# Kernel optimization log

Hardware: AMD Instinct MI355X
Metric: run time of the kernel (lower is better)

The kernel has to match this reference:

```python
import jax, jax.numpy as jnp
import numpy as np
from jax import lax

B, C_IN = 8192, 1

def _conv(x, w, b):
    # x: [N,C,H,W], w: [O,I,kh,kw] valid conv, stride 1
    y = lax.conv_general_dilated(x, w, window_strides=(1, 1), padding='VALID',
                                 dimension_numbers=('NCHW', 'OIHW', 'NCHW'))
    return y + b[None, :, None, None]

def _maxpool2(x):
    return lax.reduce_window(x, -jnp.inf, lax.max, (1, 1, 2, 2), (1, 1, 2, 2), 'VALID')

def setup_inputs() -> dict:
    key = jax.random.key(0)
    ks = jax.random.split(key, 9)
    def kaiming(k, shape, fan_in):
        return jax.random.normal(k, shape, jnp.float32) * np.float32(1.0 / np.sqrt(fan_in))
    x = jax.random.normal(ks[0], (B, C_IN, 28, 28), jnp.float32)
    w1 = kaiming(ks[1], (10, C_IN, 5, 5), C_IN * 25)
    b1 = kaiming(ks[2], (10,), C_IN * 25)
    w2 = kaiming(ks[3], (20, 10, 5, 5), 10 * 25)
    b2 = kaiming(ks[4], (20,), 10 * 25)
    wl1 = kaiming(ks[5], (50, 320), 320)
    bl1 = kaiming(ks[6], (50,), 320)
    wl2 = kaiming(ks[7], (10, 50), 50)
    bl2 = kaiming(ks[8], (10,), 50)
    return {"x": x, "w1": w1, "b1": b1, "w2": w2, "b2": b2,
            "wl1": wl1, "bl1": bl1, "wl2": wl2, "bl2": bl2}

def reference(x, w1, b1, w2, b2, wl1, bl1, wl2, bl2):
    h = jax.nn.relu(_conv(x, w1, b1))       # [B,10,24,24]
    h = _maxpool2(h)                         # [B,10,12,12]
    h = jax.nn.relu(_conv(h, w2, b2))        # [B,20,8,8]
    h = _maxpool2(h)                         # [B,20,4,4]
    h = h.reshape(h.shape[0], -1)            # [B,320]
    h = jax.nn.relu(h @ wl1.T + bl1)         # [B,50]
    return h @ wl2.T + bl2                   # [B,10]
```

## Files before the change

### kernel.cpp

```cpp
#include <hip/hip_runtime.h>

#define THREADS 256
#define IPB 4

typedef _Float16 f16;
typedef _Float16 f16x2 __attribute__((ext_vector_type(2)));
typedef _Float16 f16x8 __attribute__((ext_vector_type(8)));
typedef float f32x2 __attribute__((ext_vector_type(2)));
typedef float f32x4 __attribute__((ext_vector_type(4)));
typedef float f32x16 __attribute__((ext_vector_type(16)));
typedef unsigned int uint;

__device__ __forceinline__ f16x2 pkrtz(float a, float b) {
    return __builtin_bit_cast(f16x2, __builtin_amdgcn_cvt_pkrtz(a, b));
}
template<int CTRL>
__device__ __forceinline__ float dppmax(float v) {
    const int i = __builtin_bit_cast(int, v);
    const int s = __builtin_amdgcn_update_dpp(i, i, CTRL, 0xF, 0xF, true);
    return fmaxf(v, __builtin_bit_cast(float, s));
}

#define P1_ROW 400
#define P1_IMG 4784
#define SMEM_BYTES 19136

__global__ void pack_weights(const float* __restrict__ w1,
                             const float* __restrict__ w2,
                             const float* __restrict__ wl1,
                             unsigned char* __restrict__ ws) {
    uint* w1pk  = (uint*)ws;
    f16x8* w2af = (f16x8*)(ws + 1024);
    f16x8* wl1pk = (f16x8*)(ws + 17408);
    const int gid = blockIdx.x * blockDim.x + threadIdx.x;
    const int gsz = gridDim.x * blockDim.x;
    for (int i = gid; i < 250; i += gsz) {
        const unsigned short u =
            __builtin_bit_cast(unsigned short, (f16)w1[i]);
        w1pk[i] = (uint)u | ((uint)u << 16);
    }
    for (int e = gid; e < 1000; e += gsz) {
        const int s = e / 40, r = e - s * 40;
        const int oc = r >> 1, h = r & 1;
        f16x8 a;
        #pragma unroll
        for (int j = 0; j < 8; ++j) {
            const int ic = h * 8 + j;
            a[j] = (f16)(ic < 10 ? w2[(oc * 10 + ic) * 25 + s] : 0.f);
        }
        w2af[e] = a;
    }
    for (int e = gid; e < 2560; e += gsz) {
        const int tile = e / 640, rem = e % 640;
        const int s = rem / 64, lane = rem % 64;
        const int m = lane & 15, quad = lane >> 4;
        const int hh = tile * 16 + m;
        f16x8 a;
        #pragma unroll
        for (int j = 0; j < 8; ++j)
            a[j] = (f16)(hh < 50 ? wl1[hh * 320 + s * 32 + quad * 8 + j] : 0.f);
        wl1pk[e] = a;
    }
}

__global__ __launch_bounds__(THREADS, 8)
void lenet_one(const float* __restrict__ x,
               const unsigned char* __restrict__ ws, const float* __restrict__ b1,
               const float* __restrict__ b2,
               const float* __restrict__ bl1,
               const float* __restrict__ wl2, const float* __restrict__ bl2,
               float* __restrict__ out, int batch)
{
    __shared__ __align__(16) unsigned char p1c[SMEM_BYTES];
    f16*   p2h = (f16*)p1c;
    float* h1  = (float*)(p1c + 2624);

    const uint*  w1pk  = (const uint*)ws;
    const f16x8* w2af  = (const f16x8*)(ws + 1024);
    const f16x8* wl1pk = (const f16x8*)(ws + 17408);

    const int tid = threadIdx.x;
    const int lane = tid & 63;
    const int wv_ = tid >> 6;
    const int cM = lane & 31, hK = lane >> 5;
    const int img = tid & 3;
    const int imgg = min(blockIdx.x * IPB + img, batch - 1);

    {
        const int grp = tid >> 2;
        const float* xim = x + (size_t)imgg * 784;
        for (int pq = grp; pq < 144; pq += 64) {
            const int py = pq / 12, px = pq % 12;
            const float* xb = xim + (2 * py) * 28 + 2 * px;
            f16x2 accT[10], accB[10];
            #pragma unroll
            for (int c = 0; c < 10; ++c) {
                accT[c] = {(f16)0.f, (f16)0.f};
                accB[c] = {(f16)0.f, (f16)0.f};
            }
            #pragma unroll
            for (int r = 0; r < 6; ++r) {
                const f32x2 a01 = *(const f32x2*)(xb + r * 28);
                const f32x2 a23 = *(const f32x2*)(xb + r * 28 + 2);
                const f32x2 a45 = *(const f32x2*)(xb + r * 28 + 4);
                f16x2 p[5];
                p[0] = pkrtz(a01[0], a01[1]);
                p[1] = pkrtz(a01[1], a23[0]);
                p[2] = pkrtz(a23[0], a23[1]);
                p[3] = pkrtz(a23[1], a45[0]);
                p[4] = pkrtz(a45[0], a45[1]);
                #pragma unroll
                for (int c = 0; c < 10; ++c) {
                    #pragma unroll
                    for (int kx = 0; kx < 5; ++kx) {
                        if (r < 5) {
                            const f16x2 wv = __builtin_bit_cast(
                                f16x2, w1pk[c * 25 + r * 5 + kx]);
                            accT[c] += p[kx] * wv;
                        }
                        if (r >= 1) {
                            const f16x2 wv = __builtin_bit_cast(
                                f16x2, w1pk[c * 25 + (r - 1) * 5 + kx]);
                            accB[c] += p[kx] * wv;
                        }
                    }
                }
            }
            f16 ch[10];
            #pragma unroll
            for (int c = 0; c < 10; ++c) {
                const float q0 = fmaxf((float)accT[c][0], (float)accB[c][0]);
                const float q1 = fmaxf((float)accT[c][1], (float)accB[c][1]);
                ch[c] = (f16)fmaxf(fmaxf(q0, q1) + b1[c], 0.f);
            }
            f16x8 v0, v1;
            #pragma unroll
            for (int j = 0; j < 8; ++j) v0[j] = ch[j];
            v1[0] = ch[8]; v1[1] = ch[9];
            #pragma unroll
            for (int j = 2; j < 8; ++j) v1[j] = (f16)0.f;
            unsigned char* dst = p1c + img * P1_IMG + py * P1_ROW + px * 32;
            *(f16x8*)(dst)      = v0;
            *(f16x8*)(dst + 16) = v1;
        }
    }
    __syncthreads();

    {
        const int cy = cM >> 3, cx = cM & 7;
        const int afoff = (cM < 20 ? cM : 19) * 2 + hK;
        int bb[2];
        #pragma unroll
        for (int q = 0; q < 2; ++q) {
            const int t = wv_ * 2 + q, im = t >> 1, h2 = t & 1;
            bb[q] = im * P1_IMG + (4 * h2 + cy) * P1_ROW + cx * 32 + hK * 16;
        }
        f32x16 acc[2];
        #pragma unroll
        for (int q = 0; q < 2; ++q)
            #pragma unroll
            for (int r = 0; r < 16; ++r) acc[q][r] = 0.f;
        #pragma unroll 1
        for (int ky = 0; ky < 5; ++ky) {
            #pragma unroll
            for (int kx = 0; kx < 5; ++kx) {
                const f16x8 a = w2af[(ky * 5 + kx) * 40 + afoff];
                #pragma unroll
                for (int q = 0; q < 2; ++q) {
                    const f16x8 b =
                        *(const f16x8*)(p1c + bb[q] + ky * P1_ROW + kx * 32);
                    acc[q] = __builtin_amdgcn_mfma_f32_32x32x16_f16(a, b, acc[q],
                                                                    0, 0, 0);
                }
            }
        }
        __syncthreads();
        #pragma unroll
        for (int q = 0; q < 2; ++q) {
            const int t = wv_ * 2 + q, im = t >> 1, h2 = t & 1;
            #pragma unroll
            for (int r = 0; r < 16; ++r) {
                const int m = (r & 3) + 8 * (r >> 2) + 4 * hK;
                float v = acc[q][r];
                v = dppmax<0xB1>(v);
                v = dppmax<0x128>(v);
                if (m < 20 && (lane & 9) == 0) {
                    const int py = 2 * h2 + (cM >> 4), px = cx >> 1;
                    p2h[im * 328 + m * 16 + py * 4 + px] =
                        (f16)fmaxf(v + b2[m], 0.f);
                }
            }
        }
    }
    __syncthreads();

    {
        const int n = lane & 15, quad = lane >> 4;
        f32x4 facc = {0.f, 0.f, 0.f, 0.f};
        #pragma unroll 1
        for (int s = 0; s < 10; ++s) {
            const f16x8 a = wl1pk[(wv_ * 10 + s) * 64 + lane];
            f16x8 b = {};
            if (n < IPB)
                b = *(const f16x8*)(p2h + n * 328 + s * 32 + quad * 8);
            facc = __builtin_amdgcn_mfma_f32_16x16x32_f16(a, b, facc, 0, 0, 0);
        }
        if (n < IPB) {
            #pragma unroll
            for (int r = 0; r < 4; ++r) {
                const int h = wv_ * 16 + quad * 4 + r;
                if (h < 50)
                    h1[n * 52 + h] = fmaxf(facc[r] + bl1[h], 0.f);
            }
        }
    }
    __syncthreads();

    if (tid < IPB * 10) {
        const int im = tid / 10, o = tid % 10;
        const int imgo = min(blockIdx.x * IPB + im, batch - 1);
        float a = bl2[o];
        #pragma unroll
        for (int h = 0; h < 50; ++h)
            a += h1[im * 52 + h] * wl2[o * 50 + h];
        out[(size_t)imgo * 10 + o] = a;
    }
}

extern "C" void kernel_launch(void* const* d_in, const int* in_sizes, int n_in,
                              void* d_out, int out_size, void* d_ws, size_t ws_size,
                              hipStream_t stream) {
    const float* x   = (const float*)d_in[0];
    const float* w1  = (const float*)d_in[1];
    const float* b1  = (const float*)d_in[2];
    const float* w2  = (const float*)d_in[3];
    const float* b2  = (const float*)d_in[4];
    const float* wl1 = (const float*)d_in[5];
    const float* bl1 = (const float*)d_in[6];
    const float* wl2 = (const float*)d_in[7];
    const float* bl2 = (const float*)d_in[8];
    float* out = (float*)d_out;
    unsigned char* ws = (unsigned char*)d_ws;

    const int batch = in_sizes[0] / 784;
    pack_weights<<<64, 256, 0, stream>>>(w1, w2, wl1, ws);
    const int grid = (batch + IPB - 1) / IPB;
    lenet_one<<<grid, THREADS, 0, stream>>>(x, ws, b1, b2, bl1, wl2, bl2,
                                            out, batch);
}
```

Before: 147.6 us.

## Move conv1 onto MFMA with staged fp16 input tile and compact pool1 layout

Replaces the per-thread packed-half FMA conv1 with an MFMA 16x16x32 formulation. The input image is first staged into shared memory as fp16 overlapping pairs, and the bias is folded into the weight matrix through a ones column. The pooled conv1 output moves to a tighter 24-byte-per-pixel layout, so conv2 now reads its B operand as two 8-byte loads. Images are processed in two sub-batches of two to fit the smaller shared-memory budget. This adds extra barriers and more complex indexing in exchange for removing the long scalar-VALU conv1 loop.

Result: faster. 124.4 us (-15.7%).

```diff
diff --git a/kernel.cpp b/kernel.cpp
--- a/kernel.cpp
+++ b/kernel.cpp
@@ -5,6 +5,7 @@
 
 typedef _Float16 f16;
 typedef _Float16 f16x2 __attribute__((ext_vector_type(2)));
+typedef _Float16 f16x4 __attribute__((ext_vector_type(4)));
 typedef _Float16 f16x8 __attribute__((ext_vector_type(8)));
 typedef float f32x2 __attribute__((ext_vector_type(2)));
 typedef float f32x4 __attribute__((ext_vector_type(4)));
@@ -20,25 +21,28 @@
     const int s = __builtin_amdgcn_update_dpp(i, i, CTRL, 0xF, 0xF, true);
     return fmaxf(v, __builtin_bit_cast(float, s));
 }
-
-#define P1_ROW 400
-#define P1_IMG 4784
-#define SMEM_BYTES 19136
+__device__ __forceinline__ f16x8 ldpairs(const unsigned char* a) {
+    const uint* p = (const uint*)a;
+    uint4 u;
+    u.x = p[0]; u.y = p[2]; u.z = p[4]; u.w = p[6];
+    return __builtin_bit_cast(f16x8, u);
+}
+
+#define P1C 24
+#define P1R 288
+#define P1I 3456
+#define XH  13824
+#define XH_IMG 3136
+#define SMEM_BYTES 20224
 
 __global__ void pack_weights(const float* __restrict__ w1,
                              const float* __restrict__ w2,
                              const float* __restrict__ wl1,
                              unsigned char* __restrict__ ws) {
-    uint* w1pk  = (uint*)ws;
     f16x8* w2af = (f16x8*)(ws + 1024);
     f16x8* wl1pk = (f16x8*)(ws + 17408);
     const int gid = blockIdx.x * blockDim.x + threadIdx.x;
     const int gsz = gridDim.x * blockDim.x;
-    for (int i = gid; i < 250; i += gsz) {
-        const unsigned short u =
-            __builtin_bit_cast(unsigned short, (f16)w1[i]);
-        w1pk[i] = (uint)u | ((uint)u << 16);
-    }
     for (int e = gid; e < 1000; e += gsz) {
         const int s = e / 40, r = e - s * 40;
         const int oc = r >> 1, h = r & 1;
@@ -65,86 +69,105 @@
 
 __global__ __launch_bounds__(THREADS, 8)
 void lenet_one(const float* __restrict__ x,
-               const unsigned char* __restrict__ ws, const float* __restrict__ b1,
+               const unsigned char* __restrict__ ws,
+               const float* __restrict__ w1, const float* __restrict__ b1,
                const float* __restrict__ b2,
                const float* __restrict__ bl1,
                const float* __restrict__ wl2, const float* __restrict__ bl2,
                float* __restrict__ out, int batch)
 {
-    __shared__ __align__(16) unsigned char p1c[SMEM_BYTES];
-    f16*   p2h = (f16*)p1c;
-    float* h1  = (float*)(p1c + 2624);
-
-    const uint*  w1pk  = (const uint*)ws;
+    __shared__ __align__(16) unsigned char smem[SMEM_BYTES];
+    f16*   p2h = (f16*)smem;
+    float* h1  = (float*)(smem + 2624);
+
     const f16x8* w2af  = (const f16x8*)(ws + 1024);
     const f16x8* wl1pk = (const f16x8*)(ws + 17408);
 
     const int tid = threadIdx.x;
     const int lane = tid & 63;
     const int wv_ = tid >> 6;
+    const int n15 = lane & 15;
+    const int q4  = lane >> 4;
     const int cM = lane & 31, hK = lane >> 5;
-    const int img = tid & 3;
-    const int imgg = min(blockIdx.x * IPB + img, batch - 1);
-
-    {
-        const int grp = tid >> 2;
-        const float* xim = x + (size_t)imgg * 784;
-        for (int pq = grp; pq < 144; pq += 64) {
-            const int py = pq / 12, px = pq % 12;
-            const float* xb = xim + (2 * py) * 28 + 2 * px;
-            f16x2 accT[10], accB[10];
-            #pragma unroll
-            for (int c = 0; c < 10; ++c) {
-                accT[c] = {(f16)0.f, (f16)0.f};
-                accB[c] = {(f16)0.f, (f16)0.f};
-            }
-            #pragma unroll
-            for (int r = 0; r < 6; ++r) {
-                const f32x2 a01 = *(const f32x2*)(xb + r * 28);
-                const f32x2 a23 = *(const f32x2*)(xb + r * 28 + 2);
-                const f32x2 a45 = *(const f32x2*)(xb + r * 28 + 4);
-                f16x2 p[5];
-                p[0] = pkrtz(a01[0], a01[1]);
-                p[1] = pkrtz(a01[1], a23[0]);
-                p[2] = pkrtz(a23[0], a23[1]);
-                p[3] = pkrtz(a23[1], a45[0]);
-                p[4] = pkrtz(a45[0], a45[1]);
-                #pragma unroll
-                for (int c = 0; c < 10; ++c) {
-                    #pragma unroll
-                    for (int kx = 0; kx < 5; ++kx) {
-                        if (r < 5) {
-                            const f16x2 wv = __builtin_bit_cast(
-                                f16x2, w1pk[c * 25 + r * 5 + kx]);
-                            accT[c] += p[kx] * wv;
-                        }
-                        if (r >= 1) {
-                            const f16x2 wv = __builtin_bit_cast(
-                                f16x2, w1pk[c * 25 + (r - 1) * 5 + kx]);
-                            accB[c] += p[kx] * wv;
-                        }
-                    }
-                }
-            }
-            f16 ch[10];
-            #pragma unroll
-            for (int c = 0; c < 10; ++c) {
-                const float q0 = fmaxf((float)accT[c][0], (float)accB[c][0]);
-                const float q1 = fmaxf((float)accT[c][1], (float)accB[c][1]);
-                ch[c] = (f16)fmaxf(fmaxf(q0, q1) + b1[c], 0.f);
-            }
-            f16x8 v0, v1;
-            #pragma unroll
-            for (int j = 0; j < 8; ++j) v0[j] = ch[j];
-            v1[0] = ch[8]; v1[1] = ch[9];
-            #pragma unroll
-            for (int j = 2; j < 8; ++j) v1[j] = (f16)0.f;
-            unsigned char* dst = p1c + img * P1_IMG + py * P1_ROW + px * 32;
-            *(f16x8*)(dst)      = v0;
-            *(f16x8*)(dst + 16) = v1;
-        }
-    }
-    __syncthreads();
+
+    f16x8 A1 = {}, A2 = {};
+    if (n15 < 10) {
+        #pragma unroll
+        for (int j = 0; j < 5; ++j) A1[j] = (f16)w1[n15 * 25 + q4 * 5 + j];
+        if (q4 == 0) {
+            #pragma unroll
+            for (int j = 0; j < 5; ++j) A2[j] = (f16)w1[n15 * 25 + 20 + j];
+        }
+        if (q4 == 1) A2[0] = (f16)b1[n15];
+    }
+
+    #pragma unroll 1
+    for (int sub = 0; sub < 2; ++sub) {
+        if (tid < 112) {
+            const int imL = tid / 56, rr = (tid % 56) >> 1, half = tid & 1;
+            const int ig = min(blockIdx.x * IPB + sub * 2 + imL, batch - 1);
+            const float* xp = x + (size_t)ig * 784 + rr * 28 + half * 14;
+            float v[15];
+            #pragma unroll
+            for (int t = 0; t < 7; ++t) {
+                const f32x2 a = *(const f32x2*)(xp + 2 * t);
+                v[2 * t] = a[0]; v[2 * t + 1] = a[1];
+            }
+            v[14] = half ? 0.f : xp[14];
+            uint* pw = (uint*)(smem + XH + imL * XH_IMG + rr * 112) + half * 14;
+            #pragma unroll
+            for (int t = 0; t < 7; ++t) {
+                uint2 w;
+                w.x = __builtin_bit_cast(uint, pkrtz(v[2 * t], v[2 * t + 1]));
+                w.y = __builtin_bit_cast(uint, pkrtz(v[2 * t + 1], v[2 * t + 2]));
+                *(uint2*)(pw + 2 * t) = w;
+            }
+        } else if (tid >= 224) {
+            *(uint*)(smem + XH + 2 * XH_IMG + (tid - 224) * 4) = 0;
+        }
+        __syncthreads();
+
+        #pragma unroll 1
+        for (int i = 0; i < 12; ++i) {
+            const int g = wv_ * 12 + i;
+            const int imL = g / 24, rem = g % 24, u = rem >> 1, oxg = rem & 1;
+            const int ox = oxg * 16 + n15;
+            const unsigned char* pb = smem + XH + imL * XH_IMG + ox * 4;
+            const int oy0 = 2 * u;
+            const f16x8 B1a = ldpairs(pb + (oy0 + q4) * 112);
+            const f16x8 B1b = ldpairs(pb + (oy0 + 1 + q4) * 112);
+            f16x8 B2a = {}, B2b = {};
+            if (q4 == 0) {
+                B2a = ldpairs(pb + (oy0 + 4) * 112);
+                B2b = ldpairs(pb + (oy0 + 5) * 112);
+            } else if (q4 == 1) {
+                B2a[0] = (f16)1.f; B2b[0] = (f16)1.f;
+            }
+            f32x4 aa = {0.f, 0.f, 0.f, 0.f}, ab = {0.f, 0.f, 0.f, 0.f};
+            aa = __builtin_amdgcn_mfma_f32_16x16x32_f16(A1, B1a, aa, 0, 0, 0);
+            ab = __builtin_amdgcn_mfma_f32_16x16x32_f16(A1, B1b, ab, 0, 0, 0);
+            aa = __builtin_amdgcn_mfma_f32_16x16x32_f16(A2, B2a, aa, 0, 0, 0);
+            ab = __builtin_amdgcn_mfma_f32_16x16x32_f16(A2, B2b, ab, 0, 0, 0);
+            float vr[4];
+            #pragma unroll
+            for (int r = 0; r < 4; ++r) {
+                float v = fmaxf(aa[r], ab[r]);
+                v = dppmax<0xB1>(v);
+                vr[r] = fmaxf(v, 0.f);
+            }
+            if (!(lane & 1) && q4 < 3 && (oxg == 0 || n15 < 8)) {
+                const int im = sub * 2 + imL, px = oxg * 8 + (n15 >> 1);
+                f16x2 o0, o1;
+                o0[0] = (f16)vr[0]; o0[1] = (f16)vr[1];
+                o1[0] = (f16)vr[2]; o1[1] = (f16)vr[3];
+                uint2 w;
+                w.x = __builtin_bit_cast(uint, o0);
+                w.y = __builtin_bit_cast(uint, o1);
+                *(uint2*)(smem + im * P1I + u * P1R + px * P1C + q4 * 8) = w;
+            }
+        }
+        __syncthreads();
+    }
 
     {
         const int cy = cM >> 3, cx = cM & 7;
@@ -153,7 +176,7 @@
         #pragma unroll
         for (int q = 0; q < 2; ++q) {
             const int t = wv_ * 2 + q, im = t >> 1, h2 = t & 1;
-            bb[q] = im * P1_IMG + (4 * h2 + cy) * P1_ROW + cx * 32 + hK * 16;
+            bb[q] = im * P1I + (4 * h2 + cy) * P1R + cx * P1C + hK * 16;
         }
         f32x16 acc[2];
         #pragma unroll
@@ -167,8 +190,12 @@
                 const f16x8 a = w2af[(ky * 5 + kx) * 40 + afoff];
                 #pragma unroll
                 for (int q = 0; q < 2; ++q) {
-                    const f16x8 b =
-                        *(const f16x8*)(p1c + bb[q] + ky * P1_ROW + kx * 32);
+                    const unsigned char* ad = smem + bb[q] + ky * P1R + kx * P1C;
+                    const f16x4 lo = *(const f16x4*)(ad);
+                    const f16x4 hi = *(const f16x4*)(ad + 8);
+                    f16x8 b;
+                    #pragma unroll
+                    for (int j = 0; j < 4; ++j) { b[j] = lo[j]; b[4 + j] = hi[j]; }
                     acc[q] = __builtin_amdgcn_mfma_f32_32x32x16_f16(a, b, acc[q],
                                                                     0, 0, 0);
                 }
@@ -195,22 +222,21 @@
     __syncthreads();
 
     {
-        const int n = lane & 15, quad = lane >> 4;
         f32x4 facc = {0.f, 0.f, 0.f, 0.f};
         #pragma unroll 1
         for (int s = 0; s < 10; ++s) {
             const f16x8 a = wl1pk[(wv_ * 10 + s) * 64 + lane];
             f16x8 b = {};
-            if (n < IPB)
-                b = *(const f16x8*)(p2h + n * 328 + s * 32 + quad * 8);
+            if (n15 < IPB)
+                b = *(const f16x8*)(p2h + n15 * 328 + s * 32 + q4 * 8);
             facc = __builtin_amdgcn_mfma_f32_16x16x32_f16(a, b, facc, 0, 0, 0);
         }
-        if (n < IPB) {
+        if (n15 < IPB) {
             #pragma unroll
             for (int r = 0; r < 4; ++r) {
-                const int h = wv_ * 16 + quad * 4 + r;
+                const int h = wv_ * 16 + q4 * 4 + r;
                 if (h < 50)
-                    h1[n * 52 + h] = fmaxf(facc[r] + bl1[h], 0.f);
+                    h1[n15 * 52 + h] = fmaxf(facc[r] + bl1[h], 0.f);
             }
         }
     }
@@ -245,6 +271,6 @@
     const int batch = in_sizes[0] / 784;
     pack_weights<<<64, 256, 0, stream>>>(w1, w2, wl1, ws);
     const int grid = (batch + IPB - 1) / IPB;
-    lenet_one<<<grid, THREADS, 0, stream>>>(x, ws, b1, b2, bl1, wl2, bl2,
+    lenet_one<<<grid, THREADS, 0, stream>>>(x, ws, w1, b1, b2, bl1, wl2, bl2,
                                             out, batch);
 }
```
